# Kernel optimization log

Hardware: AMD Instinct MI355X
Metric: run time of the kernel (lower is better)

The kernel has to match this reference:

```python
import jax, jax.numpy as jnp
import numpy as np
from jax import lax

N = 56          # markers (graph nodes)
C_IN, C1, C2 = 3, 32, 64   # marker_gcn_dim = [3, 32, 64]
B, T = 32, 64   # batch, window
H = 512         # lstm hidden
OUT = 256       # output_num


def _adjacency():
    """Chain skeleton + random extra edges, symmetrized, with self loops
    (mirrors dense_to_sparse + add_self_loops on a connectivity matrix)."""
    rng = np.random.RandomState(0)
    A = np.zeros((N, N), np.float32)
    for i in range(N - 1):
        A[i, i + 1] = 1.0
    for _ in range(2 * N):
        a, b = rng.randint(0, N, 2)
        A[a, b] = 1.0
    A = np.maximum(A, A.T)
    np.fill_diagonal(A, 1.0)
    return A


def _block_mask(out_c, in_c, A):
    # mask[out_c*tgt:(tgt+1)*out_c, in_c*src:(src+1)*in_c] = 1 iff edge (src->tgt)
    return jnp.asarray(np.kron(A, np.ones((out_c, in_c), np.float32)))


def setup_inputs() -> dict:
    key = jax.random.key(0)
    ks = jax.random.split(key, 16)
    A = _adjacency()

    def w(k, shape, fan_in):
        return jax.random.normal(k, shape, jnp.float32) / np.sqrt(fan_in)

    d1_in, d1_out = C_IN * N, C1 * N      # 168, 1792
    d2_in, d2_out = C1 * N, C2 * N        # 1792, 3584
    lstm_in = C2 * N                      # 3584

    inp = {
        "x": jax.random.normal(ks[0], (B, T, d1_in), jnp.float32),
        "w1": w(ks[1], (d1_out, d1_in), d1_in),
        "b1": w(ks[2], (d1_out,), d1_in),
        "mask1": _block_mask(C1, C_IN, A),
        "w2": w(ks[3], (d2_out, d2_in), d2_in),
        "b2": w(ks[4], (d2_out,), d2_in),
        "mask2": _block_mask(C2, C1, A),
        "w_ih_f": w(ks[5], (4 * H, lstm_in), lstm_in),
        "w_hh_f": w(ks[6], (4 * H, H), H),
        "b_ih_f": w(ks[7], (4 * H,), H),
        "b_hh_f": w(ks[8], (4 * H,), H),
        "w_ih_b": w(ks[9], (4 * H, lstm_in), lstm_in),
        "w_hh_b": w(ks[10], (4 * H, H), H),
        "b_ih_b": w(ks[11], (4 * H,), H),
        "b_hh_b": w(ks[12], (4 * H,), H),
        "wo1": w(ks[13], (OUT, 2 * H), 2 * H),
        "bo1": jnp.zeros((OUT,), jnp.float32),
        "wo2": w(ks[14], (OUT, OUT), OUT),
        "bo2": jnp.zeros((OUT,), jnp.float32),
    }
    return inp


def _lstm_dir(xt, w_ih, w_hh, b, h0, c0):
    # xt: [T, B, I]; PyTorch gate order: i, f, g, o
    x_proj = jnp.einsum('tbi,gi->tbg', xt, w_ih) + b  # precompute input GEMM

    def step(carry, xp):
        h, c = carry
        g = xp + h @ w_hh.T
        i, f, gg, o = jnp.split(g, 4, axis=-1)
        c = jax.nn.sigmoid(f) * c + jax.nn.sigmoid(i) * jnp.tanh(gg)
        h = jax.nn.sigmoid(o) * jnp.tanh(c)
        return (h, c), h

    (h, c), ys = lax.scan(step, (h0, c0), x_proj)
    return ys, h, c


def _forward(x, w1, b1, mask1, w2, b2, mask2,
             w_ih_f, w_hh_f, b_ih_f, b_hh_f,
             w_ih_b, w_hh_b, b_ih_b, b_hh_b,
             wo1, bo1, wo2, bo2):
    bt = B * T
    h = x.reshape(bt, -1)
    # SkeletonLinear 1 + ReLU (edge-masked GEMM)
    h = jax.nn.relu(h @ (w1 * mask1).T + b1)
    # SkeletonLinear 2 + ReLU
    h = jax.nn.relu(h @ (w2 * mask2).T + b2)
    seq = h.reshape(B, T, -1).transpose(1, 0, 2)  # [T, B, 3584]

    h0 = jnp.zeros((B, H), x.dtype)
    c0 = jnp.zeros((B, H), x.dtype)
    yf, hf, cf = _lstm_dir(seq, w_ih_f, w_hh_f, b_ih_f + b_hh_f, h0, c0)
    yb, hb, cb = _lstm_dir(seq[::-1], w_ih_b, w_hh_b, b_ih_b + b_hh_b, h0, c0)
    y = jnp.concatenate([yf, yb[::-1]], axis=-1)  # [T, B, 2H]
    y = y.transpose(1, 0, 2).reshape(bt, 2 * H)

    # Dropout(0.5) is identity in eval mode
    o = jax.nn.relu(y @ wo1.T + bo1)
    o = o @ wo2.T + bo2
    out = o.reshape(B, T, OUT)
    hidden = jnp.stack([hf, hb])  # [2, B, H]
    c = jnp.stack([cf, cb])
    return out, hidden, c


def reference(x, w1, b1, mask1, w2, b2, mask2,
              w_ih_f, w_hh_f, b_ih_f, b_hh_f,
              w_ih_b, w_hh_b, b_ih_b, b_hh_b,
              wo1, bo1, wo2, bo2):
    return _forward(x, w1, b1, mask1, w2, b2, mask2,
                    w_ih_f, w_hh_f, b_ih_f, b_hh_f,
                    w_ih_b, w_hh_b, b_ih_b, b_hh_b,
                    wo1, bo1, wo2, bo2)
```

## Files before the change

kernel.cpp:

```cpp
#include <hip/hip_runtime.h>
#include <stddef.h>

typedef float f32x4 __attribute__((ext_vector_type(4)));
typedef short s16x8 __attribute__((ext_vector_type(8)));

__device__ __forceinline__ short f2bf(float f) {
    unsigned u = __float_as_uint(f);
    unsigned r = (u + 0x7fffu + ((u >> 16) & 1u)) >> 16;
    return (short)r;
}

__device__ __forceinline__ void load_lds16(const void* g, void* l) {
    __builtin_amdgcn_global_load_lds(
        (const __attribute__((address_space(1))) unsigned int*)g,
        (__attribute__((address_space(3))) unsigned int*)l, 16, 0, 0);
}

template<bool OBF16, bool RELU>
__global__ __launch_bounds__(256)
void gemm_mfma(const short* __restrict__ A, const short* __restrict__ W,
               const float* __restrict__ bias, void* __restrict__ Cv,
               int M, int N, int K)
{
    __shared__ short As[128 * 64];
    __shared__ short Bs[128 * 64];
    const int tid = threadIdx.x;
    const int l    = tid & 63;
    const int wave = tid >> 6;
    const int wr = wave >> 1, wc = wave & 1;

    const int nwg = gridDim.x * gridDim.y;
    const int f = blockIdx.y * gridDim.x + blockIdx.x;
    const int rank = (f & 7) * (nwg >> 3) + (f >> 3);
    const int n0 = (rank / gridDim.y) * 128;
    const int m0 = (rank % gridDim.y) * 128;

    f32x4 acc[4][4];
#pragma unroll
    for (int i = 0; i < 4; ++i)
#pragma unroll
        for (int j = 0; j < 4; ++j) {
            acc[i][j][0] = 0.f; acc[i][j][1] = 0.f;
            acc[i][j][2] = 0.f; acc[i][j][3] = 0.f;
        }

    const int srow = tid >> 3;
    const int gc   = (tid & 7) ^ (srow & 7);
    const short* gA = A + (size_t)(m0 + srow) * K + gc * 8;
    const short* gB = W + (size_t)(n0 + srow) * K + gc * 8;
    char* AsB = (char*)As;
    char* BsB = (char*)Bs;
    char* dstA = AsB + wave * 1024;
    char* dstB = BsB + wave * 1024;

    int aoff[4], boff[4], soff[2];
#pragma unroll
    for (int mi = 0; mi < 4; ++mi) aoff[mi] = (wr * 64 + mi * 16 + (l & 15)) * 128;
#pragma unroll
    for (int ni = 0; ni < 4; ++ni) boff[ni] = (wc * 64 + ni * 16 + (l & 15)) * 128;
#pragma unroll
    for (int kh = 0; kh < 2; ++kh) soff[kh] = ((kh * 4 + (l >> 4)) ^ (l & 7)) * 16;

    for (int kt = 0; kt < K; kt += 64) {
#pragma unroll
        for (int j = 0; j < 4; ++j) {
            load_lds16(gA + (size_t)j * 32 * K + kt, dstA + j * 4096);
            load_lds16(gB + (size_t)j * 32 * K + kt, dstB + j * 4096);
        }
        __syncthreads();
#pragma unroll
        for (int kh = 0; kh < 2; ++kh) {
            s16x8 af[4], bfr[4];
#pragma unroll
            for (int mi = 0; mi < 4; ++mi)
                af[mi] = *(const s16x8*)(AsB + aoff[mi] + soff[kh]);
#pragma unroll
            for (int ni = 0; ni < 4; ++ni)
                bfr[ni] = *(const s16x8*)(BsB + boff[ni] + soff[kh]);
#pragma unroll
            for (int mi = 0; mi < 4; ++mi)
#pragma unroll
                for (int ni = 0; ni < 4; ++ni)
                    acc[mi][ni] = __builtin_amdgcn_mfma_f32_16x16x32_bf16(
                        af[mi], bfr[ni], acc[mi][ni], 0, 0, 0);
        }
        __syncthreads();
    }

    const int colf = l & 15, rowf = (l >> 4) * 4;
#pragma unroll
    for (int mi = 0; mi < 4; ++mi)
#pragma unroll
        for (int ni = 0; ni < 4; ++ni) {
            const int n = n0 + wc * 64 + ni * 16 + colf;
            const float bv = bias[n];
#pragma unroll
            for (int r = 0; r < 4; ++r) {
                const int m = m0 + wr * 64 + mi * 16 + rowf + r;
                float v = acc[mi][ni][r] + bv;
                if (RELU) v = fmaxf(v, 0.f);
                if (OBF16) ((short*)Cv)[(size_t)m * N + n] = f2bf(v);
                else       ((float*)Cv)[(size_t)m * N + n] = v;
            }
        }
}

__global__ void conv_bf16(const float* __restrict__ in, const float* __restrict__ mask,
                          short* __restrict__ out, int n4)
{
    int i = blockIdx.x * blockDim.x + threadIdx.x;
    if (i >= n4) return;
    float4 v = ((const float4*)in)[i];
    if (mask) {
        float4 m = ((const float4*)mask)[i];
        v.x *= m.x; v.y *= m.y; v.z *= m.z; v.w *= m.w;
    }
    short4 o;
    o.x = f2bf(v.x); o.y = f2bf(v.y); o.z = f2bf(v.z); o.w = f2bf(v.w);
    ((short4*)out)[i] = o;
}

__global__ void padconv_bf16(const float* __restrict__ in, const float* __restrict__ mask,
                             short* __restrict__ out, int M, int Kin4, int Kout4)
{
    int idx = blockIdx.x * blockDim.x + threadIdx.x;
    if (idx >= M * Kout4) return;
    int m = idx / Kout4, k4 = idx % Kout4;
    float4 v = make_float4(0.f, 0.f, 0.f, 0.f);
    if (k4 < Kin4) {
        v = ((const float4*)in)[(size_t)m * Kin4 + k4];
        if (mask) {
            float4 mm = ((const float4*)mask)[(size_t)m * Kin4 + k4];
            v.x *= mm.x; v.y *= mm.y; v.z *= mm.z; v.w *= mm.w;
        }
    }
    short4 o;
    o.x = f2bf(v.x); o.y = f2bf(v.y); o.z = f2bf(v.z); o.w = f2bf(v.w);
    ((short4*)out)[(size_t)m * Kout4 + k4] = o;
}

__global__ void bias_sum_kernel(const float* __restrict__ bihf, const float* __restrict__ bhhf,
                                const float* __restrict__ bihb, const float* __restrict__ bhhb,
                                float* __restrict__ o)
{
    int i = blockIdx.x * blockDim.x + threadIdx.x;
    if (i < 2048)      o[i] = bihf[i] + bhhf[i];
    else if (i < 4096) o[i] = bihb[i - 2048] + bhhb[i - 2048];
}

__global__ __launch_bounds__(256, 2)
void lstm_step2(int t,
                const float* __restrict__ xp,
                const short* __restrict__ whb,
                short* __restrict__ hbuf,
                float* __restrict__ cbuf,
                short* __restrict__ y,
                float* __restrict__ out)
{
    __shared__ short wT[8 * 32 * 64];
    __shared__ short hT[8 * 32 * 64];
    __shared__ float gbuf[4][32][9];

    const int bid = blockIdx.x;
    const int dir = bid >> 6;
    const int jg  = bid & 63;
    const int j0  = jg * 8;
    const int tid = threadIdx.x;
    const int l    = tid & 63;
    const int wave = tid >> 6;
    const int tt = dir ? (63 - t) : t;

    const short* whh = whb + (size_t)dir * 1048576;
    const short* hread  = hbuf + dir * 2 * 16384 + (t & 1) * 16384;
    short*       hwrite = hbuf + dir * 2 * 16384 + ((t + 1) & 1) * 16384;
    float*       cst    = cbuf + dir * 16384;

    char* wTB = (char*)wT;
    char* hTB = (char*)hT;

    const int gb = tid >> 3;
    const int gj = tid & 7;
    const int j  = j0 + gj;

    const float* xpr = xp + ((size_t)(gb * 64 + tt)) * 4096 + dir * 2048 + j;
    const float xi = xpr[0], xf = xpr[512], xg = xpr[1024], xo = xpr[1536];
    float c_old = cst[gb * 512 + j];

    const int rloc = wave * 8 + (l >> 3);
    const int gc   = (l & 7) ^ (rloc & 7);
    const short* gW = whh + (size_t)((rloc >> 3) * 512 + j0 + (rloc & 7)) * 512 + gc * 8;
    const short* gH = hread + rloc * 512 + gc * 8;
    char* dstW = wTB + wave * 1024;
    char* dstH = hTB + wave * 1024;

#pragma unroll
    for (int kt = 0; kt < 8; ++kt) {
        load_lds16(gH + kt * 64, dstH + kt * 4096);
        load_lds16(gW + kt * 64, dstW + kt * 4096);
    }

    int soff[2];
    soff[0] = ((0 * 4 + (l >> 4)) ^ (l & 7)) * 16;
    soff[1] = ((1 * 4 + (l >> 4)) ^ (l & 7)) * 16;
    const int a0off = (l & 15) * 128;
    const int a1off = (16 + (l & 15)) * 128;
    const int bof   = (wave * 8 + (l & 7)) * 128;

    __syncthreads();

    f32x4 acc0, acc1;
    acc0[0] = 0.f; acc0[1] = 0.f; acc0[2] = 0.f; acc0[3] = 0.f;
    acc1 = acc0;
#pragma unroll
    for (int kt = 0; kt < 8; ++kt) {
#pragma unroll
        for (int kh = 0; kh < 2; ++kh) {
            s16x8 bv = *(const s16x8*)(wTB + kt * 4096 + bof + soff[kh]);
            s16x8 a0 = *(const s16x8*)(hTB + kt * 4096 + a0off + soff[kh]);
            s16x8 a1 = *(const s16x8*)(hTB + kt * 4096 + a1off + soff[kh]);
            acc0 = __builtin_amdgcn_mfma_f32_16x16x32_bf16(a0, bv, acc0, 0, 0, 0);
            acc1 = __builtin_amdgcn_mfma_f32_16x16x32_bf16(a1, bv, acc1, 0, 0, 0);
        }
    }

    if ((l & 15) < 8) {
        const int sj = l & 15, r4 = (l >> 4) * 4;
#pragma unroll
        for (int r = 0; r < 4; ++r) {
            gbuf[wave][r4 + r][sj]      = acc0[r];
            gbuf[wave][16 + r4 + r][sj] = acc1[r];
        }
    }
    __syncthreads();

    {
        float g_i = gbuf[0][gb][gj] + xi;
        float g_f = gbuf[1][gb][gj] + xf;
        float g_g = gbuf[2][gb][gj] + xg;
        float g_o = gbuf[3][gb][gj] + xo;
        float si = 1.f / (1.f + expf(-g_i));
        float sf = 1.f / (1.f + expf(-g_f));
        float so = 1.f / (1.f + expf(-g_o));
        float tg = tanhf(g_g);
        float c_new = sf * c_old + si * tg;
        float h_new = so * tanhf(c_new);

        cst[gb * 512 + j] = c_new;
        const short hb16 = f2bf(h_new);
        hwrite[gb * 512 + j] = hb16;
        y[((size_t)(gb * 64 + tt)) * 1024 + dir * 512 + j] = hb16;

        if (t == 63) {
            out[524288 + dir * 16384 + gb * 512 + j]         = h_new;
            out[524288 + 32768 + dir * 16384 + gb * 512 + j] = c_new;
        }
    }
}

extern "C" void kernel_launch(void* const* d_in, const int* in_sizes, int n_in,
                              void* d_out, int out_size, void* d_ws, size_t ws_size,
                              hipStream_t stream)
{
    const float* x     = (const float*)d_in[0];
    const float* w1    = (const float*)d_in[1];
    const float* b1    = (const float*)d_in[2];
    const float* mask1 = (const float*)d_in[3];
    const float* w2    = (const float*)d_in[4];
    const float* b2    = (const float*)d_in[5];
    const float* mask2 = (const float*)d_in[6];
    const float* wihf  = (const float*)d_in[7];
    const float* whhf  = (const float*)d_in[8];
    const float* bihf  = (const float*)d_in[9];
    const float* bhhf  = (const float*)d_in[10];
    const float* wihb  = (const float*)d_in[11];
    const float* whhb  = (const float*)d_in[12];
    const float* bihb  = (const float*)d_in[13];
    const float* bhhb  = (const float*)d_in[14];
    const float* wo1   = (const float*)d_in[15];
    const float* bo1   = (const float*)d_in[16];
    const float* wo2   = (const float*)d_in[17];
    const float* bo2   = (const float*)d_in[18];
    float* out = (float*)d_out;

    char* base = (char*)d_ws;
    short* wqb  = (short*)base;
    short* whb  = (short*)base;
    char*  Breg = base + 29360128;
    short* h2b  = (short*)Breg;
    short* xpad = (short*)Breg;
    short* w1mb = (short*)(Breg + 786432);
    char*  Creg = base + 44040192;
    float* xp   = (float*)Creg;
    short* w2b  = (short*)Creg;
    char*  Dreg = base + 77594624;
    short* h1b  = (short*)Dreg;
    short* ybuf = (short*)Dreg;
    short* o1   = (short*)(Dreg + 4194304);
    short* wo1b = (short*)(Dreg + 5242880);
    short* wo2b = (short*)(Dreg + 5767168);
    char*  Ereg = base + 84934656;
    short* hbuf = (short*)Ereg;
    float* cbuf = (float*)(Ereg + 131072);
    float* bsum = (float*)(Ereg + 262144);

    hipMemsetAsync(Ereg, 0, 262144, stream);
    bias_sum_kernel<<<16, 256, 0, stream>>>(bihf, bhhf, bihb, bhhb, bsum);

    conv_bf16<<<6272, 256, 0, stream>>>(w2, mask2, w2b, 6422528 / 4);
    conv_bf16<<<7168, 256, 0, stream>>>(wihf, nullptr, wqb, 7340032 / 4);
    conv_bf16<<<7168, 256, 0, stream>>>(wihb, nullptr, wqb + 7340032, 7340032 / 4);
    padconv_bf16<<<384, 256, 0, stream>>>(x, nullptr, xpad, 2048, 42, 48);
    padconv_bf16<<<336, 256, 0, stream>>>(w1, mask1, w1mb, 1792, 42, 48);

    gemm_mfma<true, true><<<dim3(1792 / 128, 2048 / 128), 256, 0, stream>>>(
        xpad, w1mb, b1, h1b, 2048, 1792, 192);

    gemm_mfma<true, true><<<dim3(3584 / 128, 2048 / 128), 256, 0, stream>>>(
        h1b, w2b, b2, h2b, 2048, 3584, 1792);

    gemm_mfma<false, false><<<dim3(4096 / 128, 2048 / 128), 256, 0, stream>>>(
        h2b, wqb, bsum, xp, 2048, 4096, 3584);

    conv_bf16<<<1024, 256, 0, stream>>>(whhf, nullptr, whb, 1048576 / 4);
    conv_bf16<<<1024, 256, 0, stream>>>(whhb, nullptr, whb + 1048576, 1048576 / 4);
    conv_bf16<<<256, 256, 0, stream>>>(wo1, nullptr, wo1b, 262144 / 4);
    conv_bf16<<<64, 256, 0, stream>>>(wo2, nullptr, wo2b, 65536 / 4);

    for (int t = 0; t < 64; ++t)
        lstm_step2<<<128, 256, 0, stream>>>(t, xp, whb, hbuf, cbuf, ybuf, out);

    gemm_mfma<true, true><<<dim3(256 / 128, 2048 / 128), 256, 0, stream>>>(
        ybuf, wo1b, bo1, o1, 2048, 256, 1024);
    gemm_mfma<false, false><<<dim3(256 / 128, 2048 / 128), 256, 0, stream>>>(
        o1, wo2b, bo2, out, 2048, 256, 256);
}
```

Measured before the change: 613.0 us.

## Replace per-timestep LSTM launches with persistent kernel using flag-based grid sync

The 64 separate per-timestep LSTM launches become a single persistent kernel of 128 blocks. Each block keeps its slice of W_hh resident in LDS and its cell state in registers. Blocks exchange h through global memory using atomic stores and per-block step flags, spinning until every block in the same direction has published. This removes 63 kernel launch gaps and the per-step reload of W_hh and c, but depends on all 128 blocks being co-resident and adds spin-wait cost on every step.

```diff
diff --git a/kernel.cpp b/kernel.cpp
--- a/kernel.cpp
+++ b/kernel.cpp
@@ -3,6 +3,7 @@
 
 typedef float f32x4 __attribute__((ext_vector_type(4)));
 typedef short s16x8 __attribute__((ext_vector_type(8)));
+typedef unsigned long long u64;
 
 __device__ __forceinline__ short f2bf(float f) {
     unsigned u = __float_as_uint(f);
@@ -148,18 +149,18 @@
     else if (i < 4096) o[i] = bihb[i - 2048] + bhhb[i - 2048];
 }
 
-__global__ __launch_bounds__(256, 2)
-void lstm_step2(int t,
-                const float* __restrict__ xp,
-                const short* __restrict__ whb,
-                short* __restrict__ hbuf,
-                float* __restrict__ cbuf,
-                short* __restrict__ y,
-                float* __restrict__ out)
+__global__ __launch_bounds__(256, 1)
+void lstm_persist2(const float* __restrict__ xp,
+                   const short* __restrict__ whb,
+                   short* __restrict__ hbuf,
+                   short* __restrict__ y,
+                   float* __restrict__ out,
+                   unsigned* __restrict__ flags)
 {
     __shared__ short wT[8 * 32 * 64];
     __shared__ short hT[8 * 32 * 64];
     __shared__ float gbuf[4][32][9];
+    __shared__ short hout[32][8];
 
     const int bid = blockIdx.x;
     const int dir = bid >> 6;
@@ -168,35 +169,23 @@
     const int tid = threadIdx.x;
     const int l    = tid & 63;
     const int wave = tid >> 6;
-    const int tt = dir ? (63 - t) : t;
 
     const short* whh = whb + (size_t)dir * 1048576;
-    const short* hread  = hbuf + dir * 2 * 16384 + (t & 1) * 16384;
-    short*       hwrite = hbuf + dir * 2 * 16384 + ((t + 1) & 1) * 16384;
-    float*       cst    = cbuf + dir * 16384;
+    short* hb = hbuf + dir * 2 * 16384;
+    unsigned* myflag  = flags + (size_t)(dir * 64 + jg) * 16;
+    unsigned* dirflag = flags + (size_t)dir * 1024;
 
     char* wTB = (char*)wT;
     char* hTB = (char*)hT;
 
-    const int gb = tid >> 3;
-    const int gj = tid & 7;
-    const int j  = j0 + gj;
-
-    const float* xpr = xp + ((size_t)(gb * 64 + tt)) * 4096 + dir * 2048 + j;
-    const float xi = xpr[0], xf = xpr[512], xg = xpr[1024], xo = xpr[1536];
-    float c_old = cst[gb * 512 + j];
-
-    const int rloc = wave * 8 + (l >> 3);
-    const int gc   = (l & 7) ^ (rloc & 7);
-    const short* gW = whh + (size_t)((rloc >> 3) * 512 + j0 + (rloc & 7)) * 512 + gc * 8;
-    const short* gH = hread + rloc * 512 + gc * 8;
-    char* dstW = wTB + wave * 1024;
-    char* dstH = hTB + wave * 1024;
-
-#pragma unroll
-    for (int kt = 0; kt < 8; ++kt) {
-        load_lds16(gH + kt * 64, dstH + kt * 4096);
-        load_lds16(gW + kt * 64, dstW + kt * 4096);
+    {
+        const int rloc = wave * 8 + (l >> 3);
+        const int gc   = (l & 7) ^ (rloc & 7);
+        const short* gW = whh + (size_t)((rloc >> 3) * 512 + j0 + (rloc & 7)) * 512 + gc * 8;
+        char* dstW = wTB + wave * 1024;
+#pragma unroll
+        for (int kt = 0; kt < 8; ++kt)
+            load_lds16(gW + kt * 64, dstW + kt * 4096);
     }
 
     int soff[2];
@@ -206,54 +195,108 @@
     const int a1off = (16 + (l & 15)) * 128;
     const int bof   = (wave * 8 + (l & 7)) * 128;
 
-    __syncthreads();
-
-    f32x4 acc0, acc1;
-    acc0[0] = 0.f; acc0[1] = 0.f; acc0[2] = 0.f; acc0[3] = 0.f;
-    acc1 = acc0;
-#pragma unroll
-    for (int kt = 0; kt < 8; ++kt) {
-#pragma unroll
-        for (int kh = 0; kh < 2; ++kh) {
-            s16x8 bv = *(const s16x8*)(wTB + kt * 4096 + bof + soff[kh]);
-            s16x8 a0 = *(const s16x8*)(hTB + kt * 4096 + a0off + soff[kh]);
-            s16x8 a1 = *(const s16x8*)(hTB + kt * 4096 + a1off + soff[kh]);
-            acc0 = __builtin_amdgcn_mfma_f32_16x16x32_bf16(a0, bv, acc0, 0, 0, 0);
-            acc1 = __builtin_amdgcn_mfma_f32_16x16x32_bf16(a1, bv, acc1, 0, 0, 0);
-        }
-    }
-
-    if ((l & 15) < 8) {
-        const int sj = l & 15, r4 = (l >> 4) * 4;
-#pragma unroll
-        for (int r = 0; r < 4; ++r) {
-            gbuf[wave][r4 + r][sj]      = acc0[r];
-            gbuf[wave][16 + r4 + r][sj] = acc1[r];
-        }
-    }
-    __syncthreads();
-
-    {
-        float g_i = gbuf[0][gb][gj] + xi;
-        float g_f = gbuf[1][gb][gj] + xf;
-        float g_g = gbuf[2][gb][gj] + xg;
-        float g_o = gbuf[3][gb][gj] + xo;
-        float si = 1.f / (1.f + expf(-g_i));
-        float sf = 1.f / (1.f + expf(-g_f));
-        float so = 1.f / (1.f + expf(-g_o));
-        float tg = tanhf(g_g);
-        float c_new = sf * c_old + si * tg;
-        float h_new = so * tanhf(c_new);
-
-        cst[gb * 512 + j] = c_new;
-        const short hb16 = f2bf(h_new);
-        hwrite[gb * 512 + j] = hb16;
-        y[((size_t)(gb * 64 + tt)) * 1024 + dir * 512 + j] = hb16;
-
-        if (t == 63) {
-            out[524288 + dir * 16384 + gb * 512 + j]         = h_new;
-            out[524288 + 32768 + dir * 16384 + gb * 512 + j] = c_new;
-        }
+    const int srow = wave * 8 + (l >> 3);
+    const int q    = l & 7;
+    char* hdst = hTB + q * 4096 + srow * 128;
+    const int rx = srow & 7;
+
+    const int gb = tid >> 3;
+    const int gj = tid & 7;
+    const int j  = j0 + gj;
+
+    float c_reg = 0.f;
+
+    for (int t = 0; t < 64; ++t) {
+        const int tt = dir ? (63 - t) : t;
+        const short* hread  = hb + (t & 1) * 16384;
+        short*       hwrite = hb + ((t + 1) & 1) * 16384;
+
+        const float* xpr = xp + ((size_t)(gb * 64 + tt)) * 4096 + dir * 2048 + j;
+        const float xi = xpr[0], xf = xpr[512], xg = xpr[1024], xo = xpr[1536];
+
+        {
+            const u64* hs = (const u64*)(hread + srow * 512 + q * 64);
+#pragma unroll
+            for (int p = 0; p < 8; ++p) {
+                union { u64 w[2]; s16x8 v; } u;
+                u.w[0] = __hip_atomic_load(hs + p * 2,     __ATOMIC_RELAXED, __HIP_MEMORY_SCOPE_AGENT);
+                u.w[1] = __hip_atomic_load(hs + p * 2 + 1, __ATOMIC_RELAXED, __HIP_MEMORY_SCOPE_AGENT);
+                *(s16x8*)(hdst + ((p ^ rx) << 4)) = u.v;
+            }
+        }
+        __syncthreads();
+
+        f32x4 acc0, acc1;
+        acc0[0] = 0.f; acc0[1] = 0.f; acc0[2] = 0.f; acc0[3] = 0.f;
+        acc1 = acc0;
+#pragma unroll
+        for (int kt = 0; kt < 8; ++kt) {
+#pragma unroll
+            for (int kh = 0; kh < 2; ++kh) {
+                s16x8 bv = *(const s16x8*)(wTB + kt * 4096 + bof + soff[kh]);
+                s16x8 a0 = *(const s16x8*)(hTB + kt * 4096 + a0off + soff[kh]);
+                s16x8 a1 = *(const s16x8*)(hTB + kt * 4096 + a1off + soff[kh]);
+                acc0 = __builtin_amdgcn_mfma_f32_16x16x32_bf16(a0, bv, acc0, 0, 0, 0);
+                acc1 = __builtin_amdgcn_mfma_f32_16x16x32_bf16(a1, bv, acc1, 0, 0, 0);
+            }
+        }
+
+        if ((l & 15) < 8) {
+            const int sj = l & 15, r4 = (l >> 4) * 4;
+#pragma unroll
+            for (int r = 0; r < 4; ++r) {
+                gbuf[wave][r4 + r][sj]      = acc0[r];
+                gbuf[wave][16 + r4 + r][sj] = acc1[r];
+            }
+        }
+        __syncthreads();
+
+        {
+            float g_i = gbuf[0][gb][gj] + xi;
+            float g_f = gbuf[1][gb][gj] + xf;
+            float g_g = gbuf[2][gb][gj] + xg;
+            float g_o = gbuf[3][gb][gj] + xo;
+            float si = 1.f / (1.f + expf(-g_i));
+            float sf = 1.f / (1.f + expf(-g_f));
+            float so = 1.f / (1.f + expf(-g_o));
+            float tg = tanhf(g_g);
+            c_reg = sf * c_reg + si * tg;
+            float h_new = so * tanhf(c_reg);
+
+            const short hb16 = f2bf(h_new);
+            hout[gb][gj] = hb16;
+            y[((size_t)(gb * 64 + tt)) * 1024 + dir * 512 + j] = hb16;
+
+            if (t == 63) {
+                out[524288 + dir * 16384 + gb * 512 + j]         = h_new;
+                out[524288 + 32768 + dir * 16384 + gb * 512 + j] = c_reg;
+            }
+        }
+        __syncthreads();
+
+        if (t == 63) break;
+
+        if (tid < 64) {
+            const int row = tid >> 1, seg = tid & 1;
+            union { unsigned short s[4]; u64 w; } pk;
+#pragma unroll
+            for (int i2 = 0; i2 < 4; ++i2)
+                pk.s[i2] = (unsigned short)hout[row][seg * 4 + i2];
+            __hip_atomic_store((u64*)(hwrite + row * 512 + j0 + seg * 4),
+                               pk.w, __ATOMIC_RELAXED, __HIP_MEMORY_SCOPE_AGENT);
+        }
+        if (tid == 0)
+            __hip_atomic_store(myflag, (unsigned)(t + 1),
+                               __ATOMIC_RELEASE, __HIP_MEMORY_SCOPE_AGENT);
+        if (tid < 64) {
+            for (;;) {
+                unsigned v = __hip_atomic_load(dirflag + (size_t)l * 16,
+                                               __ATOMIC_RELAXED, __HIP_MEMORY_SCOPE_AGENT);
+                if (__ballot(v >= (unsigned)(t + 1)) == ~0ull) break;
+                __builtin_amdgcn_s_sleep(2);
+            }
+        }
+        __syncthreads();
     }
 }
 
@@ -300,10 +343,10 @@
     short* wo2b = (short*)(Dreg + 5767168);
     char*  Ereg = base + 84934656;
     short* hbuf = (short*)Ereg;
-    float* cbuf = (float*)(Ereg + 131072);
-    float* bsum = (float*)(Ereg + 262144);
-
-    hipMemsetAsync(Ereg, 0, 262144, stream);
+    unsigned* flagsp = (unsigned*)(Ereg + 131072);
+    float* bsum = (float*)(Ereg + 139264);
+
+    hipMemsetAsync(Ereg, 0, 139264, stream);
     bias_sum_kernel<<<16, 256, 0, stream>>>(bihf, bhhf, bihb, bhhb, bsum);
 
     conv_bf16<<<6272, 256, 0, stream>>>(w2, mask2, w2b, 6422528 / 4);
@@ -326,8 +369,7 @@
     conv_bf16<<<256, 256, 0, stream>>>(wo1, nullptr, wo1b, 262144 / 4);
     conv_bf16<<<64, 256, 0, stream>>>(wo2, nullptr, wo2b, 65536 / 4);
 
-    for (int t = 0; t < 64; ++t)
-        lstm_step2<<<128, 256, 0, stream>>>(t, xp, whb, hbuf, cbuf, ybuf, out);
+    lstm_persist2<<<128, 256, 0, stream>>>(xp, whb, hbuf, ybuf, out, flagsp);
 
     gemm_mfma<true, true><<<dim3(256 / 128, 2048 / 128), 256, 0, stream>>>(
         ybuf, wo1b, bo1, o1, 2048, 256, 1024);
```

Measured after the change: 795.3 us. 1.3x slower.
